# Kernel optimization log

Measured on AMD Instinct MI355X. Metric: run time of the kernel, lower is better.

Reference implementation:

```python
import jax, jax.numpy as jnp
import numpy as np

F = 4        # number of factors
M = 256      # codebook size per factor
D = 8192     # hypervector dimension
B = 256      # batch of composite vectors to factorize
ITERS = 10   # resonator iterations


def setup_inputs() -> dict:
    key = jax.random.key(0)
    k1, k2 = jax.random.split(key, 2)
    # bipolar (+1/-1) codebooks, shape [F, M, D]
    cb = jnp.sign(jax.random.normal(k1, (F, M, D), dtype=jnp.float32))
    codebooks = jnp.where(cb == 0, 1.0, cb)
    # composite inputs: bind (elementwise product) of one random codevector per factor
    idx = jax.random.randint(k2, (B, F), 0, M)                       # [B, F]
    chosen = codebooks[jnp.arange(F)[None, :], idx]                  # [B, F, D]
    inp = jnp.prod(chosen, axis=1)                                   # [B, D]
    return {"input": inp, "codebooks": codebooks}


def _stage_concurrent(inp, est, codebooks):
    # est: [B, F, D]; codebooks: [F, M, D]; inp: [B, D]
    n = est.shape[1]
    # inv_others[:, f] = prod_{j != f} est[:, j]  (bipolar inverse == identity)
    inv_others = jnp.stack(
        [jnp.prod(jnp.concatenate([est[:, :f], est[:, f + 1:]], axis=1), axis=1)
         for f in range(n)], axis=1)                                  # [B, F, D]
    new_est = inp[:, None, :] * inv_others                            # bind -> [B, F, D]
    sim = jnp.einsum('bfd,fmd->bfm', new_est, codebooks)              # similarity
    # activation == 'NONE'
    out = jnp.einsum('bfm,fmd->bfd', sim, codebooks)                  # dot_similarity
    return jnp.sign(out)


def reference(input, codebooks):
    Bn = input.shape[0]
    # init estimates = multiset (sum) of each codebook, broadcast over batch
    init = jnp.broadcast_to(jnp.sum(codebooks, axis=1)[None], (Bn, F, D)).astype(input.dtype)

    def cond(state):
        _, k, done = state
        return jnp.logical_and(k < ITERS, jnp.logical_not(done))

    def body(state):
        est, k, _ = state
        new = _stage_concurrent(input, est, codebooks)
        return (new, k + 1, jnp.all(new == est))

    est, k, _ = jax.lax.while_loop(cond, body, (init, jnp.int32(0), jnp.array(False)))
    # cleanup: nearest codevector per factor (argmax similarity)
    sim = jnp.einsum('bfd,fmd->bfm', est, codebooks)
    outcome = jnp.argmax(sim, axis=-1)                                # [B, F] indices
    return outcome, k
```

## Files before the change

kernel.cpp:

```cpp
#include <hip/hip_runtime.h>

#define B_SZ 256
#define F_SZ 4
#define M_SZ 256
#define D_SZ 8192
#define NITER 10

typedef signed char i8;
typedef unsigned long long u64;
typedef signed char c16 __attribute__((ext_vector_type(16)));
typedef int v4i __attribute__((ext_vector_type(4)));

#define NBFM (B_SZ * F_SZ * M_SZ)

#define OFF_CB    ((size_t)0)
#define OFF_CBT   ((size_t)8  << 20)
#define OFF_IN8   ((size_t)16 << 20)
#define OFF_CBBT  ((size_t)18 << 20)
#define OFF_INB   ((size_t)19 << 20)
#define OFF_ESB   ((size_t)20 << 20)
#define OFF_EZB   ((size_t)21 << 20)
#define OFF_SIMX  ((size_t)22 << 20)
#define OFF_P1    ((size_t)23 << 20)
#define OFF_S32   ((size_t)48 << 20)
#define OFF_PDIG  (OFF_S32 + (size_t)F_SZ * D_SZ * 4)
#define OFF_CHG   (OFF_PDIG + (size_t)3 * F_SZ * D_SZ)


__global__ __launch_bounds__(256) void k_cvt_cb(const float* __restrict__ src,
                                                i8* __restrict__ cb, i8* __restrict__ cbt) {
  __shared__ i8 tile[32][33];
  const int bid = blockIdx.x;
  const int f = bid >> 11;
  const int rem = bid & 2047;
  const int m0 = (rem >> 8) << 5;
  const int d0 = (rem & 255) << 5;
  const int t = threadIdx.x;
  const int i = t >> 3, j = (t & 7) << 2;
  const float4 v = *(const float4*)(src + ((size_t)(f * M_SZ + m0 + i)) * D_SZ + d0 + j);
  char4 c;
  c.x = v.x > 0.f ? 1 : -1;
  c.y = v.y > 0.f ? 1 : -1;
  c.z = v.z > 0.f ? 1 : -1;
  c.w = v.w > 0.f ? 1 : -1;
  *(char4*)(cb + ((size_t)(f * M_SZ + m0 + i)) * D_SZ + d0 + j) = c;
  tile[i][j + 0] = c.x; tile[i][j + 1] = c.y; tile[i][j + 2] = c.z; tile[i][j + 3] = c.w;
  __syncthreads();
  const int dd = t >> 3, jm = (t & 7) << 2;
  char4 o;
  o.x = tile[jm + 0][dd]; o.y = tile[jm + 1][dd]; o.z = tile[jm + 2][dd]; o.w = tile[jm + 3][dd];
  *(char4*)(cbt + ((size_t)(f * D_SZ + d0 + dd)) * M_SZ + m0 + jm) = o;
}

__global__ __launch_bounds__(256) void k_cvt_in(const float* __restrict__ src, i8* __restrict__ dst) {
  const int idx = blockIdx.x * 256 + threadIdx.x;
  const float4 v = ((const float4*)src)[idx];
  char4 c;
  c.x = v.x > 0.f ? 1 : -1;
  c.y = v.y > 0.f ? 1 : -1;
  c.z = v.z > 0.f ? 1 : -1;
  c.w = v.w > 0.f ? 1 : -1;
  ((char4*)dst)[idx] = c;
}

__global__ __launch_bounds__(256) void k_pack_cb(const i8* __restrict__ cb, u64* __restrict__ cbbT) {
  const int id = blockIdx.x * 256 + threadIdx.x;
  const int f = id >> 15;
  const int rem = id & 32767;
  const int w = rem >> 8;
  const int m = rem & 255;
  const i8* src = cb + ((size_t)(f * M_SZ + m)) * D_SZ + w * 64;
  u64 r = 0;
  #pragma unroll
  for (int k = 0; k < 4; ++k) {
    c16 v = *(const c16*)(src + k * 16);
    u64 part = 0;
    #pragma unroll
    for (int j = 0; j < 16; ++j) part |= ((u64)(((unsigned char)v[j]) >> 7)) << j;
    r |= part << (k * 16);
  }
  cbbT[((size_t)(f * 128 + w)) * 256 + m] = r;
}

__global__ __launch_bounds__(256) void k_pack_in(const i8* __restrict__ in8, u64* __restrict__ inb) {
  const int id = blockIdx.x * 256 + threadIdx.x;
  const int b = id >> 7;
  const int w = id & 127;
  const i8* src = in8 + (size_t)b * D_SZ + w * 64;
  u64 r = 0;
  #pragma unroll
  for (int k = 0; k < 4; ++k) {
    c16 v = *(const c16*)(src + k * 16);
    u64 part = 0;
    #pragma unroll
    for (int j = 0; j < 16; ++j) part |= ((u64)(((unsigned char)v[j]) >> 7)) << j;
    r |= part << (k * 16);
  }
  inb[(size_t)b * 128 + w] = r;
}

__global__ __launch_bounds__(256) void k_S(const i8* __restrict__ cb, int* __restrict__ S) {
  const int id = blockIdx.x * 256 + threadIdx.x;
  const int f = id >> 13, d = id & 8191;
  const i8* p = cb + (size_t)f * M_SZ * D_SZ + d;
  int s = 0;
  for (int m = 0; m < M_SZ; ++m) s += p[(size_t)m * D_SZ];
  S[id] = s;
}

__global__ __launch_bounds__(256) void k_P(const int* __restrict__ S, i8* __restrict__ pdig) {
  const int d = blockIdx.x * 256 + threadIdx.x;
  const int s0 = S[d], s1 = S[D_SZ + d], s2 = S[2 * D_SZ + d], s3 = S[3 * D_SZ + d];
  int P[4];
  P[0] = s1 * s2 * s3;
  P[1] = s0 * s2 * s3;
  P[2] = s0 * s1 * s3;
  P[3] = s0 * s1 * s2;
  for (int f = 0; f < 4; ++f) {
    int x = P[f] >> 3;
    #pragma unroll
    for (int p = 0; p < 2; ++p) {
      const int y = x + 127;
      const int q = (y >= 0) ? (y / 255) : -((-y + 254) / 255);
      const int dg = x - q * 255;
      pdig[((size_t)(p * F_SZ + f)) * D_SZ + d] = (i8)dg;
      x = q;
    }
    pdig[((size_t)(2 * F_SZ + f)) * D_SZ + d] = (i8)x;
  }
}


__global__ __launch_bounds__(256) void ga2_kernel(
    const i8* __restrict__ in8, const i8* __restrict__ cb,
    const i8* __restrict__ pdig, int* __restrict__ p1)
{
  __shared__ __align__(16) i8 lA[64 * 48];
  __shared__ __align__(16) i8 lB[128 * 48];

  const int bid = blockIdx.x;
  const int s = bid & 7;
  const int r = bid >> 3;
  const int p = r % 3;
  const int q = r / 3;
  const int f = q & 3;
  const int ct = q >> 2;
  const int b0 = (ct >> 1) * 64;
  const int m0 = (ct & 1) * 128;
  const int ksteps = 32;
  const int kbase = s << 10;

  const int t = threadIdx.x;
  const int lane = t & 63;
  const int wv = t >> 6;
  const int wrow = (wv >> 1) * 32;
  const int wcol = (wv & 1) * 64;

  const int arow = t >> 1;
  const int aoff = (t & 1) * 16;
  const i8* pB  = cb   + ((size_t)(f * M_SZ + m0 + arow)) * D_SZ + aoff;
  const i8* pDg = pdig + ((size_t)(p * F_SZ + f)) * D_SZ + aoff;
  const i8* pIn = in8  + (size_t)(b0 + arow) * D_SZ + aoff;

  v4i acc[2][4];
  #pragma unroll
  for (int tr = 0; tr < 2; ++tr)
    #pragma unroll
    for (int tc = 0; tc < 4; ++tc) acc[tr][tc] = 0;

  c16 va = 0, vb = 0;
  {
    const int kk = kbase;
    vb = (*(const c16*)(pB + kk)) * (*(const c16*)(pDg + kk));
    if (t < 128) va = *(const c16*)(pIn + kk);
  }

  for (int j = 0; j < ksteps; ++j) {
    c16 sa = va, sb = vb;
    if (j + 1 < ksteps) {
      const int kk = kbase + (j + 1) * 32;
      vb = (*(const c16*)(pB + kk)) * (*(const c16*)(pDg + kk));
      if (t < 128) va = *(const c16*)(pIn + kk);
    }
    __syncthreads();
    if (t < 128) *(c16*)&lA[arow * 48 + aoff] = sa;
    *(c16*)&lB[arow * 48 + aoff] = sb;
    __syncthreads();

    const int rsel = lane & 15;
    const int kq = (lane >> 4) * 8;
    long af[2], bf[4];
    #pragma unroll
    for (int tr = 0; tr < 2; ++tr) af[tr] = *(const long*)&lA[(wrow + tr * 16 + rsel) * 48 + kq];
    #pragma unroll
    for (int tc = 0; tc < 4; ++tc) bf[tc] = *(const long*)&lB[(wcol + tc * 16 + rsel) * 48 + kq];
    #pragma unroll
    for (int tr = 0; tr < 2; ++tr)
      #pragma unroll
      for (int tc = 0; tc < 4; ++tc)
        acc[tr][tc] = __builtin_amdgcn_mfma_i32_16x16x32_i8(af[tr], bf[tc], acc[tr][tc], 0, 0, 0);
  }

  const int colb = lane & 15;
  const int rowq = (lane >> 4) * 4;
  const size_t obase = (size_t)(p * 8 + s) * NBFM;
  #pragma unroll
  for (int tr = 0; tr < 2; ++tr)
    #pragma unroll
    for (int tc = 0; tc < 4; ++tc)
      #pragma unroll
      for (int rr = 0; rr < 4; ++rr) {
        const int b = b0 + wrow + tr * 16 + rowq + rr;
        const int m = m0 + wcol + tc * 16 + colb;
        p1[obase + (((size_t)(b * F_SZ + f)) << 8) + m] = acc[tr][tc][rr];
      }
}

__global__ __launch_bounds__(256) void k_digits1(const int* __restrict__ p1, i8* __restrict__ simx) {
  const int idx = blockIdx.x * 256 + threadIdx.x;
  long long g[3];
  #pragma unroll
  for (int p = 0; p < 3; ++p) {
    long long gg = 0;
    #pragma unroll
    for (int s = 0; s < 8; ++s) gg += (long long)p1[(size_t)(p * 8 + s) * NBFM + idx];
    g[p] = gg;
  }
  const long long sim = g[0] + 255LL * g[1] + 65025LL * g[2];
  int x = (int)sim;
  const int r1 = (x + 128) >> 8;
  const int d0 = x - (r1 << 8);
  const int r2 = (r1 + 128) >> 8;
  const int d1 = r1 - (r2 << 8);
  const size_t bf = (size_t)(idx >> 8);
  const int m = idx & 255;
  simx[bf * 768 + m] = (i8)d0;
  simx[bf * 768 + 256 + m] = (i8)d1;
  simx[bf * 768 + 512 + m] = (i8)r2;
}


__global__ __launch_bounds__(512) void ga_bit(
    const u64* __restrict__ esb, const u64* __restrict__ ezb,
    const u64* __restrict__ inb, const u64* __restrict__ cbbT,
    i8* __restrict__ simx, const int* __restrict__ changed, int it)
{
  __shared__ u64 AL[128][4];
  __shared__ int C0[2];

  if (changed[it - 1] == 0) return;

  const int bid = blockIdx.x;
  const int f = bid & 3;
  const int b0 = (bid >> 2) * 2;
  const int t = threadIdx.x;
  if (t < 2) C0[t] = 0;
  __syncthreads();

  if (t < 256) {
    const int r = t >> 7, w = t & 127;
    const int b = b0 + r;
    int ffs[3]; int c = 0;
    for (int ff = 0; ff < 4; ++ff) if (ff != f) ffs[c++] = ff;
    const size_t base = (size_t)b * 4 * 128;
    const u64 s = inb[(size_t)b * 128 + w]
      ^ esb[base + ffs[0] * 128 + w] ^ esb[base + ffs[1] * 128 + w] ^ esb[base + ffs[2] * 128 + w];
    const u64 nz = ~(ezb[base + ffs[0] * 128 + w] | ezb[base + ffs[1] * 128 + w] | ezb[base + ffs[2] * 128 + w]);
    AL[w][r * 2] = s;
    AL[w][r * 2 + 1] = nz;
    int pcv = (int)__popcll(nz);
    #pragma unroll
    for (int off = 32; off >= 1; off >>= 1) pcv += __shfl_down(pcv, off);
    if ((t & 63) == 0) atomicAdd(&C0[r], pcv);
  }
  __syncthreads();

  const int r = t >> 8;
  const int m = t & 255;
  int a = 0;
  const u64* pc = cbbT + (size_t)f * 128 * 256 + m;
  #pragma unroll 8
  for (int w = 0; w < 128; ++w) {
    const u64 cbw = pc[w * 256];
    a += (int)__popcll((AL[w][r * 2] ^ cbw) & AL[w][r * 2 + 1]);
  }
  const int sim = C0[r] - 2 * a;

  const int d1 = (sim + 128) >> 8;
  const int d0v = sim - (d1 << 8);
  const size_t bf0 = ((size_t)(b0 + r) * 4 + f) * 768;
  simx[bf0 + m] = (i8)d0v;
  simx[bf0 + 256 + m] = (i8)d1;
}


template<int NP, bool FIRST>
__global__ __launch_bounds__(256) void gb_kernel(
    const i8* __restrict__ simx, const i8* __restrict__ cbt,
    u64* __restrict__ esb, u64* __restrict__ ezb,
    const int* __restrict__ S32,
    int* __restrict__ changed, int it)
{
  constexpr int LASTR = NP * 256 + 8;
  __shared__ __align__(16) i8 lB[8 * 8 * 64 * 8];
  __shared__ __align__(16) i8 lA[64 * LASTR];
  __shared__ int chgf;

  if (!FIRST) { if (changed[it - 1] == 0) return; }

  const int bid = blockIdx.x;
  const int f = bid & 3;
  const int ct = bid >> 2;
  const int b0 = (ct >> 6) * 64;
  const int d0 = (ct & 63) * 128;

  const int t = threadIdx.x;
  if (t == 0) chgf = 0;
  const int lane = t & 63;
  const int wv = t >> 6;
  const int wrow = (wv >> 1) * 32;
  const int wcol = (wv & 1) * 64;

  {
    constexpr int CPR = NP * 16;
    #pragma unroll
    for (int idx = 0; idx < 64 * CPR; idx += 256) {
      const int id = idx + t;
      const int row = id / CPR;
      const int c = id - row * CPR;
      union { c16 v; u64 u[2]; } x;
      x.v = *(const c16*)(simx + ((size_t)((b0 + row) * 4 + f)) * 768 + c * 16);
      *(u64*)&lA[row * LASTR + c * 16] = x.u[0];
      *(u64*)&lA[row * LASTR + c * 16 + 8] = x.u[1];
    }
  }
  {
    const int c = t & 15;
    const int dr0 = t >> 4;
    const int ks = c >> 1;
    const int q0 = (c & 1) * 2;
    const int swz = ((ks << 1) | (q0 >> 1)) << 3;
    #pragma unroll
    for (int i = 0; i < 8; ++i) {
      const int dr = dr0 + i * 16;
      union { c16 v; u64 u[2]; } x;
      x.v = *(const c16*)(cbt + ((size_t)(f * D_SZ + d0 + dr)) * M_SZ + c * 16);
      const int tile = dr >> 4;
      const int col = dr & 15;
      *(u64*)&lB[(((((ks * 8 + tile) * 4 + q0) * 16 + col)) * 8) ^ swz] = x.u[0];
      *(u64*)&lB[(((((ks * 8 + tile) * 4 + q0 + 1) * 16 + col)) * 8) ^ swz] = x.u[1];
    }
  }
  __syncthreads();

  v4i acc[NP][2][4];
  #pragma unroll
  for (int pp = 0; pp < NP; ++pp)
    #pragma unroll
    for (int tr = 0; tr < 2; ++tr)
      #pragma unroll
      for (int tc = 0; tc < 4; ++tc) acc[pp][tr][tc] = 0;

  const int rsel = lane & 15;
  const int kq = (lane >> 4) * 8;
  const int tb = wcol >> 4;

  #pragma unroll
  for (int ks = 0; ks < 8; ++ks) {
    const int rswz = ((ks << 1) | (lane >> 5)) << 3;
    long bf[4];
    #pragma unroll
    for (int tc = 0; tc < 4; ++tc)
      bf[tc] = *(const long*)&lB[((((ks * 8 + tb + tc) * 64 + lane)) * 8) ^ rswz];
    long af[NP][2];
    #pragma unroll
    for (int pp = 0; pp < NP; ++pp)
      #pragma unroll
      for (int tr = 0; tr < 2; ++tr)
        af[pp][tr] = *(const long*)&lA[(wrow + tr * 16 + rsel) * LASTR + pp * 256 + ks * 32 + kq];
    #pragma unroll
    for (int pp = 0; pp < NP; ++pp)
      #pragma unroll
      for (int tr = 0; tr < 2; ++tr)
        #pragma unroll
        for (int tc = 0; tc < 4; ++tc)
          acc[pp][tr][tc] = __builtin_amdgcn_mfma_i32_16x16x32_i8(af[pp][tr], bf[tc], acc[pp][tr][tc], 0, 0, 0);
  }

  bool chl = false;
  const int colb = lane & 15;

  #pragma unroll
  for (int tr = 0; tr < 2; ++tr) {
    unsigned long long bs[4][4], bz[4][4];
    #pragma unroll
    for (int rr = 0; rr < 4; ++rr)
      #pragma unroll
      for (int tc = 0; tc < 4; ++tc) {
        int o = acc[0][tr][tc][rr];
        if (NP > 1) o += acc[1][tr][tc][rr] * 256;
        if (NP > 2) o += acc[2][tr][tc][rr] * 65536;
        bs[rr][tc] = __ballot(o < 0);
        bz[rr][tc] = __ballot(o == 0);
        if (FIRST) {
          const int sg = (o > 0) - (o < 0);
          const int d = d0 + wcol + tc * 16 + colb;
          chl |= (sg != S32[f * D_SZ + d]);
        }
      }
    u64 ws = 0, wz = 0;
    #pragma unroll
    for (int rl = 0; rl < 16; ++rl) {
      const int g = rl >> 2, rr = rl & 3;
      u64 vs = 0, vz = 0;
      #pragma unroll
      for (int tc = 0; tc < 4; ++tc) {
        vs |= ((bs[rr][tc] >> (g * 16)) & 0xFFFFull) << (tc * 16);
        vz |= ((bz[rr][tc] >> (g * 16)) & 0xFFFFull) << (tc * 16);
      }
      if (lane == rl) { ws = vs; wz = vz; }
    }
    if (lane < 16) {
      const int row = b0 + wrow + tr * 16 + lane;
      const size_t wi = ((size_t)(row * 4 + f)) * 128 + ((d0 + wcol) >> 6);
      if (!FIRST) chl |= (ws != esb[wi]) | (wz != ezb[wi]);
      esb[wi] = ws;
      ezb[wi] = wz;
    }
  }
  if (chl) atomicOr(&chgf, 1);
  __syncthreads();
  if (t == 0 && chgf) atomicOr(&changed[it], 1);
}


__global__ __launch_bounds__(512) void k_final(
    const u64* __restrict__ esb, const u64* __restrict__ ezb,
    const u64* __restrict__ cbbT, const int* __restrict__ chg,
    int* __restrict__ out)
{
  __shared__ u64 AL[128][4];
  __shared__ int C0[2];
  __shared__ long long red[2][256];

  const int bid = blockIdx.x;
  const int f = bid & 3;
  const int b0 = (bid >> 2) * 2;
  const int t = threadIdx.x;
  if (t < 2) C0[t] = 0;
  __syncthreads();

  if (t < 256) {
    const int r = t >> 7, w = t & 127;
    const int b = b0 + r;
    const size_t a = ((size_t)b * 4 + f) * 128 + w;
    const u64 s = esb[a];
    const u64 nz = ~ezb[a];
    AL[w][r * 2] = s;
    AL[w][r * 2 + 1] = nz;
    int pcv = (int)__popcll(nz);
    #pragma unroll
    for (int off = 32; off >= 1; off >>= 1) pcv += __shfl_down(pcv, off);
    if ((t & 63) == 0) atomicAdd(&C0[r], pcv);
  }
  __syncthreads();

  const int r = t >> 8;
  const int m = t & 255;
  int a = 0;
  const u64* pc = cbbT + (size_t)f * 128 * 256 + m;
  #pragma unroll 8
  for (int w = 0; w < 128; ++w) {
    const u64 cbw = pc[w * 256];
    a += (int)__popcll((AL[w][r * 2] ^ cbw) & AL[w][r * 2 + 1]);
  }
  const int sim = C0[r] - 2 * a;

  red[r][m] = ((long long)sim << 32) | (long long)(unsigned)(255 - m);
  __syncthreads();
  for (int s2 = 128; s2 > 0; s2 >>= 1) {
    if (m < s2) {
      if (red[r][m + s2] > red[r][m]) red[r][m] = red[r][m + s2];
    }
    __syncthreads();
  }
  if (m == 0) {
    out[(b0 + r) * 4 + f] = 255 - (int)(red[r][0] & 0xFFFF);
    if (t == 0 && bid == 0) {
      int k = NITER;
      for (int i = 1; i <= NITER; ++i) if (chg[i] == 0) { k = i; break; }
      out[B_SZ * F_SZ] = k;
    }
  }
}


extern "C" void kernel_launch(void* const* d_in, const int* in_sizes, int n_in,
                              void* d_out, int out_size, void* d_ws, size_t ws_size,
                              hipStream_t stream) {
  const float* f_in = (const float*)d_in[0];
  const float* f_cb = (const float*)d_in[1];
  int* out = (int*)d_out;
  char* ws = (char*)d_ws;

  i8*  cb8  = (i8*)(ws + OFF_CB);
  i8*  cbt8 = (i8*)(ws + OFF_CBT);
  i8*  in8  = (i8*)(ws + OFF_IN8);
  u64* cbbT = (u64*)(ws + OFF_CBBT);
  u64* inb  = (u64*)(ws + OFF_INB);
  u64* esb  = (u64*)(ws + OFF_ESB);
  u64* ezb  = (u64*)(ws + OFF_EZB);
  i8*  simx = (i8*)(ws + OFF_SIMX);
  int* p1   = (int*)(ws + OFF_P1);
  int* S32  = (int*)(ws + OFF_S32);
  i8*  pdig = (i8*)(ws + OFF_PDIG);
  int* chg  = (int*)(ws + OFF_CHG);

  hipMemsetAsync(chg, 0, 64, stream);
  k_cvt_cb<<<dim3(8192), dim3(256), 0, stream>>>(f_cb, cb8, cbt8);
  k_cvt_in<<<dim3(2048), dim3(256), 0, stream>>>(f_in, in8);
  k_pack_cb<<<dim3(512), dim3(256), 0, stream>>>(cb8, cbbT);
  k_pack_in<<<dim3(128), dim3(256), 0, stream>>>(in8, inb);
  k_S<<<dim3(128), dim3(256), 0, stream>>>(cb8, S32);
  k_P<<<dim3(32), dim3(256), 0, stream>>>(S32, pdig);

  ga2_kernel<<<dim3(768), dim3(256), 0, stream>>>(in8, cb8, pdig, p1);
  k_digits1<<<dim3(1024), dim3(256), 0, stream>>>(p1, simx);
  gb_kernel<3, true><<<dim3(1024), dim3(256), 0, stream>>>(
      simx, cbt8, esb, ezb, S32, chg, 1);

  for (int it = 2; it <= NITER; ++it) {
    ga_bit<<<dim3(512), dim3(512), 0, stream>>>(esb, ezb, inb, cbbT, simx, chg, it);
    gb_kernel<2, false><<<dim3(1024), dim3(256), 0, stream>>>(
        simx, cbt8, esb, ezb, nullptr, chg, it);
  }

  k_final<<<dim3(512), dim3(512), 0, stream>>>(esb, ezb, cbbT, chg, out);
}
```

Baseline: 538.2 us.

## Pre-swizzle MFMA operands in global memory and drop LDS staging in gb kernel

The codebook transpose and the similarity digits are now written directly in an MFMA-fragment-ordered layout (cbF, aF01/aF2), so the gb kernel loads A and B fragments straight from global memory into registers. The shared-memory staging, swizzling and __syncthreads are removed, and change detection uses a wave-level __any with a global atomic instead of a block-wide LDS flag. Launch bounds now request higher occupancy. The trade-off is that operand reuse across waves moves from LDS to L1/L2 caches, and writes from the producer kernels become more scattered.

```diff
diff --git a/kernel.cpp b/kernel.cpp
--- a/kernel.cpp
+++ b/kernel.cpp
@@ -14,21 +14,27 @@
 #define NBFM (B_SZ * F_SZ * M_SZ)
 
 #define OFF_CB    ((size_t)0)
-#define OFF_CBT   ((size_t)8  << 20)
+#define OFF_CBF   ((size_t)8  << 20)
 #define OFF_IN8   ((size_t)16 << 20)
 #define OFF_CBBT  ((size_t)18 << 20)
 #define OFF_INB   ((size_t)19 << 20)
 #define OFF_ESB   ((size_t)20 << 20)
 #define OFF_EZB   ((size_t)21 << 20)
-#define OFF_SIMX  ((size_t)22 << 20)
+#define OFF_AF01  ((size_t)22 << 20)
+#define OFF_AF2   (OFF_AF01 + ((size_t)512 << 10))
 #define OFF_P1    ((size_t)23 << 20)
 #define OFF_S32   ((size_t)48 << 20)
 #define OFF_PDIG  (OFF_S32 + (size_t)F_SZ * D_SZ * 4)
 #define OFF_CHG   (OFF_PDIG + (size_t)3 * F_SZ * D_SZ)
 
+__device__ __forceinline__ size_t afslot(int f, int b, int m) {
+  return (size_t)(((f * 4 + (b >> 6)) * 8 + (m >> 5)) * 4 + ((b >> 4) & 3)) * 64
+         + ((m >> 3) & 3) * 16 + (b & 15);
+}
+
 
 __global__ __launch_bounds__(256) void k_cvt_cb(const float* __restrict__ src,
-                                                i8* __restrict__ cb, i8* __restrict__ cbt) {
+                                                i8* __restrict__ cb, i8* __restrict__ cbF) {
   __shared__ i8 tile[32][33];
   const int bid = blockIdx.x;
   const int f = bid >> 11;
@@ -46,10 +52,18 @@
   *(char4*)(cb + ((size_t)(f * M_SZ + m0 + i)) * D_SZ + d0 + j) = c;
   tile[i][j + 0] = c.x; tile[i][j + 1] = c.y; tile[i][j + 2] = c.z; tile[i][j + 3] = c.w;
   __syncthreads();
-  const int dd = t >> 3, jm = (t & 7) << 2;
-  char4 o;
-  o.x = tile[jm + 0][dd]; o.y = tile[jm + 1][dd]; o.z = tile[jm + 2][dd]; o.w = tile[jm + 3][dd];
-  *(char4*)(cbt + ((size_t)(f * D_SZ + d0 + dd)) * M_SZ + m0 + jm) = o;
+  if (t < 128) {
+    const int mg = t >> 5;
+    const int dd = t & 31;
+    const int d = d0 + dd;
+    const int dt = d >> 7, dsub = (d >> 4) & 7, dlo = d & 15;
+    const int ks = m0 >> 5;
+    u64 w = 0;
+    #pragma unroll
+    for (int jj = 0; jj < 8; ++jj)
+      w |= ((u64)(unsigned char)tile[mg * 8 + jj][dd]) << (8 * jj);
+    *(u64*)&cbF[((size_t)((((f * 64 + dt) * 8 + ks) * 8 + dsub) * 64 + mg * 16 + dlo)) * 8] = w;
+  }
 }
 
 __global__ __launch_bounds__(256) void k_cvt_in(const float* __restrict__ src, i8* __restrict__ dst) {
@@ -216,7 +230,8 @@
       }
 }
 
-__global__ __launch_bounds__(256) void k_digits1(const int* __restrict__ p1, i8* __restrict__ simx) {
+__global__ __launch_bounds__(256) void k_digits1(const int* __restrict__ p1,
+                                                 i8* __restrict__ aF01, i8* __restrict__ aF2) {
   const int idx = blockIdx.x * 256 + threadIdx.x;
   long long g[3];
   #pragma unroll
@@ -232,18 +247,21 @@
   const int d0 = x - (r1 << 8);
   const int r2 = (r1 + 128) >> 8;
   const int d1 = r1 - (r2 << 8);
-  const size_t bf = (size_t)(idx >> 8);
+  const int bf = idx >> 8;
   const int m = idx & 255;
-  simx[bf * 768 + m] = (i8)d0;
-  simx[bf * 768 + 256 + m] = (i8)d1;
-  simx[bf * 768 + 512 + m] = (i8)r2;
+  const int b = bf >> 2, f = bf & 3;
+  const size_t sl = afslot(f, b, m);
+  const int by = m & 7;
+  aF01[sl * 16 + by] = (i8)d0;
+  aF01[sl * 16 + 8 + by] = (i8)d1;
+  aF2[sl * 8 + by] = (i8)r2;
 }
 
 
 __global__ __launch_bounds__(512) void ga_bit(
     const u64* __restrict__ esb, const u64* __restrict__ ezb,
     const u64* __restrict__ inb, const u64* __restrict__ cbbT,
-    i8* __restrict__ simx, const int* __restrict__ changed, int it)
+    i8* __restrict__ aF01, const int* __restrict__ changed, int it)
 {
   __shared__ u64 AL[128][4];
   __shared__ int C0[2];
@@ -288,70 +306,39 @@
 
   const int d1 = (sim + 128) >> 8;
   const int d0v = sim - (d1 << 8);
-  const size_t bf0 = ((size_t)(b0 + r) * 4 + f) * 768;
-  simx[bf0 + m] = (i8)d0v;
-  simx[bf0 + 256 + m] = (i8)d1;
+  const int b = b0 + r;
+  const size_t sl = afslot(f, b, m);
+  const int by = m & 7;
+  aF01[sl * 16 + by] = (i8)d0v;
+  aF01[sl * 16 + 8 + by] = (i8)d1;
 }
 
 
 template<int NP, bool FIRST>
-__global__ __launch_bounds__(256) void gb_kernel(
-    const i8* __restrict__ simx, const i8* __restrict__ cbt,
+__device__ __forceinline__ void gb_body(
+    const i8* __restrict__ aF01, const i8* __restrict__ aF2,
+    const i8* __restrict__ cbF,
     u64* __restrict__ esb, u64* __restrict__ ezb,
     const int* __restrict__ S32,
     int* __restrict__ changed, int it)
 {
-  constexpr int LASTR = NP * 256 + 8;
-  __shared__ __align__(16) i8 lB[8 * 8 * 64 * 8];
-  __shared__ __align__(16) i8 lA[64 * LASTR];
-  __shared__ int chgf;
-
   if (!FIRST) { if (changed[it - 1] == 0) return; }
 
   const int bid = blockIdx.x;
   const int f = bid & 3;
   const int ct = bid >> 2;
-  const int b0 = (ct >> 6) * 64;
-  const int d0 = (ct & 63) * 128;
+  const int bt = ct >> 6;
+  const int dt = ct & 63;
+  const int b0 = bt * 64;
+  const int d0 = dt * 128;
 
   const int t = threadIdx.x;
-  if (t == 0) chgf = 0;
   const int lane = t & 63;
   const int wv = t >> 6;
   const int wrow = (wv >> 1) * 32;
   const int wcol = (wv & 1) * 64;
-
-  {
-    constexpr int CPR = NP * 16;
-    #pragma unroll
-    for (int idx = 0; idx < 64 * CPR; idx += 256) {
-      const int id = idx + t;
-      const int row = id / CPR;
-      const int c = id - row * CPR;
-      union { c16 v; u64 u[2]; } x;
-      x.v = *(const c16*)(simx + ((size_t)((b0 + row) * 4 + f)) * 768 + c * 16);
-      *(u64*)&lA[row * LASTR + c * 16] = x.u[0];
-      *(u64*)&lA[row * LASTR + c * 16 + 8] = x.u[1];
-    }
-  }
-  {
-    const int c = t & 15;
-    const int dr0 = t >> 4;
-    const int ks = c >> 1;
-    const int q0 = (c & 1) * 2;
-    const int swz = ((ks << 1) | (q0 >> 1)) << 3;
-    #pragma unroll
-    for (int i = 0; i < 8; ++i) {
-      const int dr = dr0 + i * 16;
-      union { c16 v; u64 u[2]; } x;
-      x.v = *(const c16*)(cbt + ((size_t)(f * D_SZ + d0 + dr)) * M_SZ + c * 16);
-      const int tile = dr >> 4;
-      const int col = dr & 15;
-      *(u64*)&lB[(((((ks * 8 + tile) * 4 + q0) * 16 + col)) * 8) ^ swz] = x.u[0];
-      *(u64*)&lB[(((((ks * 8 + tile) * 4 + q0 + 1) * 16 + col)) * 8) ^ swz] = x.u[1];
-    }
-  }
-  __syncthreads();
+  const int tb = wcol >> 4;
+  const int sub0 = wrow >> 4;
 
   v4i acc[NP][2][4];
   #pragma unroll
@@ -361,23 +348,25 @@
       #pragma unroll
       for (int tc = 0; tc < 4; ++tc) acc[pp][tr][tc] = 0;
 
-  const int rsel = lane & 15;
-  const int kq = (lane >> 4) * 8;
-  const int tb = wcol >> 4;
+  const i8* pA = aF01 + ((size_t)(f * 4 + bt)) * 8 * 4 * 64 * 16;
+  const i8* pB = cbF + ((size_t)(f * 64 + dt)) * 8 * 8 * 64 * 8;
+  const i8* pA2 = aF2 + ((size_t)(f * 4 + bt)) * 8 * 4 * 64 * 8;
 
   #pragma unroll
   for (int ks = 0; ks < 8; ++ks) {
-    const int rswz = ((ks << 1) | (lane >> 5)) << 3;
     long bf[4];
     #pragma unroll
     for (int tc = 0; tc < 4; ++tc)
-      bf[tc] = *(const long*)&lB[((((ks * 8 + tb + tc) * 64 + lane)) * 8) ^ rswz];
+      bf[tc] = *(const long*)(pB + ((size_t)((ks * 8 + tb + tc) * 64 + lane)) * 8);
     long af[NP][2];
     #pragma unroll
-    for (int pp = 0; pp < NP; ++pp)
-      #pragma unroll
-      for (int tr = 0; tr < 2; ++tr)
-        af[pp][tr] = *(const long*)&lA[(wrow + tr * 16 + rsel) * LASTR + pp * 256 + ks * 32 + kq];
+    for (int tr = 0; tr < 2; ++tr) {
+      union { c16 v; long l[2]; } x;
+      x.v = *(const c16*)(pA + ((size_t)((ks * 4 + sub0 + tr) * 64 + lane)) * 16);
+      af[0][tr] = x.l[0];
+      af[1][tr] = x.l[1];
+      if (NP > 2) af[2][tr] = *(const long*)(pA2 + ((size_t)((ks * 4 + sub0 + tr) * 64 + lane)) * 8);
+    }
     #pragma unroll
     for (int pp = 0; pp < NP; ++pp)
       #pragma unroll
@@ -428,9 +417,23 @@
       ezb[wi] = wz;
     }
   }
-  if (chl) atomicOr(&chgf, 1);
-  __syncthreads();
-  if (t == 0 && chgf) atomicOr(&changed[it], 1);
+  if (__any(chl)) { if (lane == 0) atomicOr(&changed[it], 1); }
+}
+
+__global__ __launch_bounds__(256, 4) void gb_loop(
+    const i8* __restrict__ aF01, const i8* __restrict__ cbF,
+    u64* __restrict__ esb, u64* __restrict__ ezb,
+    int* __restrict__ changed, int it)
+{
+  gb_body<2, false>(aF01, nullptr, cbF, esb, ezb, nullptr, changed, it);
+}
+
+__global__ __launch_bounds__(256, 2) void gb_first(
+    const i8* __restrict__ aF01, const i8* __restrict__ aF2, const i8* __restrict__ cbF,
+    u64* __restrict__ esb, u64* __restrict__ ezb,
+    const int* __restrict__ S32, int* __restrict__ changed, int it)
+{
+  gb_body<3, true>(aF01, aF2, cbF, esb, ezb, S32, changed, it);
 }
 
 
@@ -504,20 +507,21 @@
   char* ws = (char*)d_ws;
 
   i8*  cb8  = (i8*)(ws + OFF_CB);
-  i8*  cbt8 = (i8*)(ws + OFF_CBT);
+  i8*  cbF  = (i8*)(ws + OFF_CBF);
   i8*  in8  = (i8*)(ws + OFF_IN8);
   u64* cbbT = (u64*)(ws + OFF_CBBT);
   u64* inb  = (u64*)(ws + OFF_INB);
   u64* esb  = (u64*)(ws + OFF_ESB);
   u64* ezb  = (u64*)(ws + OFF_EZB);
-  i8*  simx = (i8*)(ws + OFF_SIMX);
+  i8*  aF01 = (i8*)(ws + OFF_AF01);
+  i8*  aF2  = (i8*)(ws + OFF_AF2);
   int* p1   = (int*)(ws + OFF_P1);
   int* S32  = (int*)(ws + OFF_S32);
   i8*  pdig = (i8*)(ws + OFF_PDIG);
   int* chg  = (int*)(ws + OFF_CHG);
 
   hipMemsetAsync(chg, 0, 64, stream);
-  k_cvt_cb<<<dim3(8192), dim3(256), 0, stream>>>(f_cb, cb8, cbt8);
+  k_cvt_cb<<<dim3(8192), dim3(256), 0, stream>>>(f_cb, cb8, cbF);
   k_cvt_in<<<dim3(2048), dim3(256), 0, stream>>>(f_in, in8);
   k_pack_cb<<<dim3(512), dim3(256), 0, stream>>>(cb8, cbbT);
   k_pack_in<<<dim3(128), dim3(256), 0, stream>>>(in8, inb);
@@ -525,14 +529,12 @@
   k_P<<<dim3(32), dim3(256), 0, stream>>>(S32, pdig);
 
   ga2_kernel<<<dim3(768), dim3(256), 0, stream>>>(in8, cb8, pdig, p1);
-  k_digits1<<<dim3(1024), dim3(256), 0, stream>>>(p1, simx);
-  gb_kernel<3, true><<<dim3(1024), dim3(256), 0, stream>>>(
-      simx, cbt8, esb, ezb, S32, chg, 1);
+  k_digits1<<<dim3(1024), dim3(256), 0, stream>>>(p1, aF01, aF2);
+  gb_first<<<dim3(1024), dim3(256), 0, stream>>>(aF01, aF2, cbF, esb, ezb, S32, chg, 1);
 
   for (int it = 2; it <= NITER; ++it) {
-    ga_bit<<<dim3(512), dim3(512), 0, stream>>>(esb, ezb, inb, cbbT, simx, chg, it);
-    gb_kernel<2, false><<<dim3(1024), dim3(256), 0, stream>>>(
-        simx, cbt8, esb, ezb, nullptr, chg, it);
+    ga_bit<<<dim3(512), dim3(512), 0, stream>>>(esb, ezb, inb, cbbT, aF01, chg, it);
+    gb_loop<<<dim3(1024), dim3(256), 0, stream>>>(aF01, cbF, esb, ezb, chg, it);
   }
 
   k_final<<<dim3(512), dim3(512), 0, stream>>>(esb, ezb, cbbT, chg, out);
```

Measured after the change: 896.1 us. 1.67x slower.
